# Kernel optimization log

Hardware: AMD Instinct MI355X
Metric: run time of the kernel (lower is better)

Reference implementation:

```python
import jax, jax.numpy as jnp
import numpy as np

B, S, I, H, C = 32, 512, 768, 512, 10


def setup_inputs() -> dict:
    key = jax.random.key(0)
    ks = jax.random.split(key, 16)
    n = lambda k, shp, s=0.02: jax.random.normal(k, shp, dtype=jnp.float32) * s
    inp = {
        "sentence_embeds": jax.random.normal(ks[0], (B, S, I), dtype=jnp.float32),
        "Wenc": n(ks[1], (H, I)),
        "benc": jnp.zeros((H,), jnp.float32),
        "Wdec": n(ks[2], (H, H)),
        "bdec": jnp.zeros((H,), jnp.float32),
        "v": jax.random.uniform(ks[3], (H,), dtype=jnp.float32),
        "Wih_f": n(ks[4], (4 * H, 2 * I)),
        "Whh_f": n(ks[5], (4 * H, H)),
        "bih_f": jnp.zeros((4 * H,), jnp.float32),
        "bhh_f": jnp.zeros((4 * H,), jnp.float32),
        "Wih_b": n(ks[6], (4 * H, 2 * I)),
        "Whh_b": n(ks[7], (4 * H, H)),
        "bih_b": jnp.zeros((4 * H,), jnp.float32),
        "bhh_b": jnp.zeros((4 * H,), jnp.float32),
        "Wout": n(ks[8], (C, 2 * H)),
        "bout": jnp.zeros((C,), jnp.float32),
    }
    return inp


def _run_direction(embeds, enc_proj, Wdec, bdec, v, Wih, Whh, bih, bhh):
    # embeds: [B,S,I], enc_proj: [B,S,H]. Returns per-step hidden states [S,B,H].
    b = embeds.shape[0]
    h0 = jnp.zeros((b, H), embeds.dtype)
    c0 = jnp.zeros((b, H), embeds.dtype)

    def step(carry, x_t):
        h, c = carry
        # Bahdanau additive attention over all encoder positions
        dec = h @ Wdec.T + bdec                                   # [B,H]
        scores = jnp.einsum("h,bsh->bs", v, jnp.tanh(enc_proj + dec[:, None, :]))
        w = jax.nn.softmax(scores, axis=1)                        # [B,S]
        ctx = jnp.einsum("bs,bsi->bi", w, embeds)                 # [B,I]
        inp = jnp.concatenate([ctx, x_t], axis=1)                 # [B,2I]
        gates = inp @ Wih.T + h @ Whh.T + (bih + bhh)             # [B,4H]
        i, f, g, o = jnp.split(gates, 4, axis=1)                  # torch LSTM gate order
        c = jax.nn.sigmoid(f) * c + jax.nn.sigmoid(i) * jnp.tanh(g)
        h = jax.nn.sigmoid(o) * jnp.tanh(c)
        return (h, c), h

    xs = jnp.swapaxes(embeds, 0, 1)  # [S,B,I]
    _, hs = jax.lax.scan(step, (h0, c0), xs)
    return hs


def reference(sentence_embeds, Wenc, benc, Wdec, bdec, v, Wih_f, Whh_f, bih_f, bhh_f,
              Wih_b, Whh_b, bih_b, bhh_b, Wout, bout):
    # Encoder projection is loop-invariant in the original; compute once.
    enc_proj = sentence_embeds @ Wenc.T + benc  # [B,S,H]
    hs_f = _run_direction(sentence_embeds, enc_proj, Wdec, bdec, v, Wih_f, Whh_f, bih_f, bhh_f)
    hs_b = _run_direction(sentence_embeds[:, ::-1, :], enc_proj, Wdec, bdec, v, Wih_b, Whh_b, bih_b, bhh_b)
    hs_b = hs_b[::-1]                                             # align backward outputs to time order
    combined = jnp.concatenate([hs_f, hs_b], axis=-1)             # [S,B,2H]
    preds = combined @ Wout.T + bout                              # [S,B,C]
    return jnp.swapaxes(preds, 0, 1)                              # [B,S,C]
```

## Files before the change

kernel.cpp:

```cpp
#include <hip/hip_runtime.h>
#include <stdint.h>

#define DEVINL __device__ __forceinline__

constexpr int B_  = 32;
constexpr int S_  = 512;
constexpr int I_  = 768;
constexpr int H_  = 512;
constexpr int C_  = 10;
constexpr int R_  = 64;
constexpr int G4H = 2048;
constexpr int I2_ = 1536;
constexpr int NBLK = 256;
constexpr int NTHR = 512;

using bf16x8 = __attribute__((ext_vector_type(8))) short;
using f32x4  = __attribute__((ext_vector_type(4))) float;
typedef unsigned short u16;
typedef unsigned int   u32;

constexpr size_t OFF_TE   = 0;
constexpr size_t OFF_EMB  = OFF_TE   + (size_t)B_*S_*H_*2;
constexpr size_t OFF_WDEC = OFF_EMB  + (size_t)B_*S_*I_*2;
constexpr size_t OFF_WHH  = OFF_WDEC + (size_t)H_*H_*2;
constexpr size_t OFF_WIL  = OFF_WHH  + (size_t)2*G4H*H_*2;
constexpr size_t OFF_WIR  = OFF_WIL  + (size_t)2*G4H*I_*2;
constexpr size_t OFF_WENC = OFF_WIR  + (size_t)2*G4H*I_*2;
constexpr size_t OFF_H    = OFF_WENC + (size_t)H_*I_*2;
constexpr size_t OFF_C    = OFF_H    + (size_t)R_*H_*2;
constexpr size_t OFF_TD   = OFF_C    + (size_t)R_*H_*4;
constexpr size_t OFF_HWH  = OFF_TD   + (size_t)R_*H_*4;
constexpr size_t OFF_XW   = OFF_HWH  + (size_t)R_*G4H*4;
constexpr size_t OFF_CTX  = OFF_XW   + (size_t)R_*G4H*4;
constexpr size_t OFF_SUME = OFF_CTX  + (size_t)R_*I_*4;
constexpr size_t OFF_M    = OFF_SUME + 256;
constexpr size_t OFF_BAR  = OFF_M    + 256;
constexpr int    BAR_W    = 64 + NBLK*32;
constexpr size_t WS_NEED  = OFF_BAR + BAR_W*4;

DEVINL float asf(u32 u){ union{u32 i; float f;} x; x.i=u; return x.f; }
DEVINL u32   asu(float f){ union{u32 i; float f;} x; x.f=f; return x.i; }
DEVINL float bf2f(u16 h){ return asf((u32)h << 16); }
DEVINL u16   f2bf(float f){ u32 u = asu(f); return (u16)((u + 0x7fffu + ((u>>16)&1u)) >> 16); }
DEVINL float frcp(float x){
#if __has_builtin(__builtin_amdgcn_rcpf)
  return __builtin_amdgcn_rcpf(x);
#else
  return 1.0f/x;
#endif
}
DEVINL float sigm(float x){ return frcp(1.0f + __expf(-x)); }

DEVINL float ldc_f(const float* p){ return __hip_atomic_load(p, __ATOMIC_RELAXED, __HIP_MEMORY_SCOPE_AGENT); }
DEVINL void  stc_f(float* p, float v){ __hip_atomic_store(p, v, __ATOMIC_RELAXED, __HIP_MEMORY_SCOPE_AGENT); }
DEVINL u32   ldc_u(const u32* p){ return __hip_atomic_load(p, __ATOMIC_RELAXED, __HIP_MEMORY_SCOPE_AGENT); }
DEVINL void  stc_u(u32* p, u32 v){ __hip_atomic_store(p, v, __ATOMIC_RELAXED, __HIP_MEMORY_SCOPE_AGENT); }
DEVINL void  addc_f(float* p, float v){ __hip_atomic_fetch_add(p, v, __ATOMIC_RELAXED, __HIP_MEMORY_SCOPE_AGENT); }

DEVINL void gridbar(u32* bar, u32 n){
  __syncthreads();
  if (threadIdx.x == 0)
    stc_u(&bar[64 + blockIdx.x*32], n);
  if (blockIdx.x == 0){
    if (threadIdx.x < NBLK){
      while (ldc_u(&bar[64 + threadIdx.x*32]) < n)
        __builtin_amdgcn_s_sleep(1);
    }
    __syncthreads();
    if (threadIdx.x == 0) stc_u(&bar[32], n);
  } else {
    if (threadIdx.x == 0){
      while (ldc_u(&bar[32]) < n)
        __builtin_amdgcn_s_sleep(1);
    }
  }
  __syncthreads();
}

DEVINL f32x4 gemm_h16(const u32* h32, size_t base, const u16 (*W)[520], int lr, int lkb){
  f32x4 acc = {0.f,0.f,0.f,0.f};
  #pragma unroll
  for (int half = 0; half < 2; ++half){
    u32 hreg[32];
    #pragma unroll
    for (int i2 = 0; i2 < 32; ++i2)
      hreg[i2] = ldc_u(h32 + base + half*128 + (i2>>2)*16 + (i2&3));
    #pragma unroll
    for (int ki = 0; ki < 8; ++ki){
      union { bf16x8 v; u32 w[4]; } ua;
      ua.w[0]=hreg[ki*4+0]; ua.w[1]=hreg[ki*4+1];
      ua.w[2]=hreg[ki*4+2]; ua.w[3]=hreg[ki*4+3];
      bf16x8 b = *(const bf16x8*)(&W[lr][(half*8+ki)*32 + lkb]);
      acc = __builtin_amdgcn_mfma_f32_16x16x32_bf16(ua.v, b, acc, 0, 0, 0);
    }
  }
  return acc;
}

struct SMemB { float ldsE[2][2][32]; float cpart[4][96][16]; };
struct SMemC { u16 Abuf[16][776]; float Gpre[32][16]; float Gs[32][16];
               float Hb[16][8]; float inv[16]; float sum[16]; };
union alignas(16) SMem { SMemB b; SMemC c; };

__global__ void k_setup(char* ws, const float* Wenc, const float* Wdec,
                        const float* Whh_f, const float* Whh_b,
                        const float* Wih_f, const float* Wih_b,
                        float* out){
  int tid = blockIdx.x*blockDim.x + threadIdx.x;
  int nth = gridDim.x*blockDim.x;
  for (int i = tid; i < B_*S_*C_; i += nth) out[i] = 0.f;
  u16* hB = (u16*)(ws+OFF_H);
  for (int i = tid; i < R_*H_; i += nth) hB[i] = 0;
  float* cS = (float*)(ws+OFF_C);
  for (int i = tid; i < R_*H_; i += nth) cS[i] = 0.f;
  float* mb = (float*)(ws+OFF_M);
  for (int i = tid; i < R_; i += nth) mb[i] = 0.f;
  u32* bar = (u32*)(ws+OFF_BAR);
  for (int i = tid; i < BAR_W; i += nth) bar[i] = 0u;
  u16* wd = (u16*)(ws+OFF_WDEC);
  for (int i = tid; i < H_*H_; i += nth) wd[i] = f2bf(Wdec[i]);
  u16* we = (u16*)(ws+OFF_WENC);
  for (int i = tid; i < H_*I_; i += nth) we[i] = f2bf(Wenc[i]);
  u16* wh = (u16*)(ws+OFF_WHH);
  for (int i = tid; i < G4H*H_; i += nth){
    wh[i] = f2bf(Whh_f[i]);
    wh[G4H*H_ + i] = f2bf(Whh_b[i]);
  }
  u16* wl = (u16*)(ws+OFF_WIL);
  u16* wr = (u16*)(ws+OFF_WIR);
  for (int i = tid; i < G4H*I_; i += nth){
    int n = i / I_, k = i - n*I_;
    wl[i]            = f2bf(Wih_f[n*I2_ + k]);
    wr[i]            = f2bf(Wih_f[n*I2_ + I_ + k]);
    wl[G4H*I_ + i]   = f2bf(Wih_b[n*I2_ + k]);
    wr[G4H*I_ + i]   = f2bf(Wih_b[n*I2_ + I_ + k]);
  }
}

__global__ void k_embconv(char* ws, const float* emb){
  u16* e = (u16*)(ws+OFF_EMB);
  int tid = blockIdx.x*blockDim.x + threadIdx.x;
  int nth = gridDim.x*blockDim.x;
  int n4 = (B_*S_*I_)/4;
  const float4* src = (const float4*)emb;
  ushort4* dst = (ushort4*)e;
  for (int i = tid; i < n4; i += nth){
    float4 x = src[i];
    ushort4 o;
    o.x = f2bf(x.x); o.y = f2bf(x.y); o.z = f2bf(x.z); o.w = f2bf(x.w);
    dst[i] = o;
  }
}

__global__ __launch_bounds__(256) void k_enc(char* ws, const float* benc){
  const u16* A = (const u16*)(ws+OFF_EMB);
  const u16* W = (const u16*)(ws+OFF_WENC);
  u16* Te = (u16*)(ws+OFF_TE);
  int wg = blockIdx.x;
  int mt = wg >> 3, ng = wg & 7;
  int wave = threadIdx.x >> 6, lane = threadIdx.x & 63;
  int m0 = mt*16, n0 = ng*64 + wave*16;
  int lr = lane & 15, lkb = (lane>>4)*8;
  const u16* ap = A + (size_t)(m0+lr)*I_ + lkb;
  const u16* bp = W + (size_t)(n0+lr)*I_ + lkb;
  f32x4 acc = {0.f,0.f,0.f,0.f};
  for (int k = 0; k < I_; k += 32){
    bf16x8 a = *(const bf16x8*)(ap + k);
    bf16x8 b = *(const bf16x8*)(bp + k);
    acc = __builtin_amdgcn_mfma_f32_16x16x32_bf16(a, b, acc, 0, 0, 0);
  }
  int row4 = (lane>>4)*4;
  #pragma unroll
  for (int q = 0; q < 4; q++){
    int rr = m0 + row4 + q, cc = n0 + lr;
    Te[(size_t)rr*H_ + cc] = f2bf(tanhf(acc[q] + benc[cc]));
  }
}

__global__ __launch_bounds__(NTHR) void k_persist(char* ws,
        const float* bdec, const float* v,
        const float* bih_f, const float* bhh_f,
        const float* bih_b, const float* bhh_b,
        const float* Wout, const float* bout, float* out){
  __shared__ SMem sh;
  __shared__ alignas(16) u16 wWhh[16][520];
  __shared__ alignas(16) u16 wWIR[16][776];
  __shared__ alignas(16) u16 wDec[16][520];
  __shared__ alignas(16) u16 wWIL[32][776];
  __shared__ float wOutL[10][8];
  __shared__ float bsumL[32];
  u32* bar = (u32*)(ws+OFF_BAR);
  u32 gen = 0;
  const int tid = threadIdx.x, lane = tid & 63, wave = tid >> 6;
  const int lr = lane & 15, lkb = (lane>>4)*8, row4 = (lane>>4)*4;
  const int blk = blockIdx.x;
  const int dirA = blk & 1, n0A = blk >> 1;
  const int ab   = blk & 31, pair = blk >> 5;
  const int s0A  = pair*32, s0B = S_ - pair*32 - 32;
  const int h0   = lane*8;
  const int cg   = (tid < 384) ? (tid % 96) : 0;
  const int rq   = (tid < 384) ? (tid / 96) : 0;
  const int dirC = blk >> 7, ncC = (blk >> 1) & 63, qbC = blk & 1;

  { const u16* src = (const u16*)(ws+OFF_WHH) + (size_t)dirA*G4H*H_ + (size_t)n0A*16*H_;
    for (int idx = tid; idx < 16*64; idx += NTHR){ int r = idx>>6, c8 = idx&63;
      *(uint4*)&wWhh[r][c8*8] = *(const uint4*)(src + (size_t)r*H_ + c8*8); } }
  { const u16* src = (const u16*)(ws+OFF_WIR) + (size_t)dirA*G4H*I_ + (size_t)n0A*16*I_;
    for (int idx = tid; idx < 16*96; idx += NTHR){ int r = idx/96, c8 = idx - r*96;
      *(uint4*)&wWIR[r][c8*8] = *(const uint4*)(src + (size_t)r*I_ + c8*8); } }
  if (blk < 32){
    const u16* src = (const u16*)(ws+OFF_WDEC) + (size_t)blk*16*H_;
    for (int idx = tid; idx < 16*64; idx += NTHR){ int r = idx>>6, c8 = idx&63;
      *(uint4*)&wDec[r][c8*8] = *(const uint4*)(src + (size_t)r*H_ + c8*8); } }
  { const u16* src = (const u16*)(ws+OFF_WIL) + (size_t)dirC*G4H*I_;
    for (int idx = tid; idx < 32*96; idx += NTHR){ int pr = idx/96, c8 = idx - pr*96;
      int g = pr>>3, j = pr&7;
      *(uint4*)&wWIL[pr][c8*8] = *(const uint4*)(src + (size_t)(g*512 + ncC*8 + j)*I_ + c8*8); } }
  { const float* bihp = dirC ? bih_b : bih_f;
    const float* bhhp = dirC ? bhh_b : bhh_f;
    if (tid < 32){ int g = tid>>3, c = tid&7; int n = g*512 + ncC*8 + c;
      bsumL[tid] = bihp[n] + bhhp[n]; }
    if (tid >= 64 && tid < 144){ int q = tid-64; int cc = q>>3, c = q&7;
      wOutL[cc][c] = Wout[(size_t)cc*1024 + dirC*512 + ncC*8 + c]; } }
  bf16x8 teR[8];
  { const u16* Te = (const u16*)(ws+OFF_TE);
    #pragma unroll
    for (int k = 0; k < 8; ++k){
      int r = wave + 8*k; int ci = r >> 5, u = r & 31;
      int s = (ci ? s0B : s0A) + u;
      teR[k] = *(const bf16x8*)(Te + ((size_t)(ab*S_ + s))*H_ + h0); } }
  bf16x8 embR[16];
  if (tid < 384){
    const u16* E = (const u16*)(ws+OFF_EMB);
    #pragma unroll
    for (int j = 0; j < 16; ++j){
      int r = rq*16 + j;
      int s = (r < 32) ? (s0A + r) : (s0B + (r - 32));
      embR[j] = *(const bf16x8*)(E + ((size_t)(ab*S_ + s))*I_ + cg*8); } }
  __syncthreads();

  for (int t = 0; t < S_; ++t){
    {
      const u32* h32 = (const u32*)(ws+OFF_H);
      if (wave < 2){
        int m0 = dirA*32 + wave*16;
        size_t base = (((size_t)(m0+lr))*H_ + lkb) >> 1;
        f32x4 acc = gemm_h16(h32, base, wWhh, lr, lkb);
        float* o = (float*)(ws+OFF_HWH);
        #pragma unroll
        for (int q = 0; q < 4; q++)
          stc_f(&o[(size_t)(m0 + row4 + q)*G4H + n0A*16 + lr], acc[q]);
      } else if (wave < 4){
        int bbase = (wave-2)*16;
        int trow = dirA ? (S_-1-t) : t;
        const u16* E = (const u16*)(ws+OFF_EMB);
        const u16* ap = E + ((size_t)(bbase+lr)*S_ + trow)*I_ + lkb;
        f32x4 acc = {0.f,0.f,0.f,0.f};
        for (int k = 0; k < I_; k += 32){
          bf16x8 a = *(const bf16x8*)(ap + k);
          bf16x8 b = *(const bf16x8*)(&wWIR[lr][k + lkb]);
          acc = __builtin_amdgcn_mfma_f32_16x16x32_bf16(a, b, acc, 0, 0, 0);
        }
        float* o = (float*)(ws+OFF_XW);
        #pragma unroll
        for (int q = 0; q < 4; q++)
          stc_f(&o[(size_t)(dirA*32 + bbase + row4 + q)*G4H + n0A*16 + lr], acc[q]);
      } else if (blk < 32){
        int m0 = (wave-4)*16;
        size_t base = (((size_t)(m0+lr))*H_ + lkb) >> 1;
        f32x4 acc = gemm_h16(h32, base, wDec, lr, lkb);
        float* Td = (float*)(ws+OFF_TD);
        #pragma unroll
        for (int q = 0; q < 4; q++){
          int rr = m0 + row4 + q, cc = blk*16 + lr;
          stc_f(&Td[rr*H_ + cc], tanhf(acc[q] + bdec[cc]));
        }
      } else {
        int zid = (((blk-32)<<2) + (wave-4))*64 + lane;
        float* ctx = (float*)(ws+OFF_CTX);
        if (zid < R_*I_) stc_f(&ctx[zid], 0.f);
        if (zid < R_) stc_f((float*)(ws+OFF_SUME) + zid, 0.f);
      }
    }
    gridbar(bar, ++gen);
    {
      const float* Td = (const float*)(ws+OFF_TD);
      const float* mbp = (const float*)(ws+OFF_M);
      float tdf[8], tdb[8], va[8];
      #pragma unroll
      for (int j = 0; j < 8; j++){
        tdf[j] = ldc_f(&Td[ab*H_ + h0 + j]);
        tdb[j] = ldc_f(&Td[(32+ab)*H_ + h0 + j]);
        va[j]  = v[h0 + j];
      }
      float mF = ldc_f(&mbp[ab]), mB = ldc_f(&mbp[32+ab]);
      #pragma unroll
      for (int k = 0; k < 8; ++k){
        int r = wave + 8*k;
        int ci = r >> 5, u = r & 31;
        bf16x8 tv = teR[k];
        float af = 0.f, ab2 = 0.f;
        #pragma unroll
        for (int j = 0; j < 8; ++j){
          float te = bf2f((u16)tv[j]);
          float df = fmaf(te, tdf[j], 1.0f);
          float db = fmaf(te, tdb[j], 1.0f);
          af  = fmaf((te+tdf[j])*frcp(df), va[j], af);
          ab2 = fmaf((te+tdb[j])*frcp(db), va[j], ab2);
        }
        #pragma unroll
        for (int off = 1; off < 64; off <<= 1){
          af  += __shfl_xor(af, off);
          ab2 += __shfl_xor(ab2, off);
        }
        float ef = __expf(fminf(fmaxf(af  - mF, -80.f), 80.f));
        float eb = __expf(fminf(fmaxf(ab2 - mB, -80.f), 80.f));
        if (lane == 0){ sh.b.ldsE[0][ci][u] = ef; sh.b.ldsE[1][ci][u] = eb; }
      }
      __syncthreads();
      if (tid < 2){
        float s = 0.f;
        for (int ci = 0; ci < 2; ci++)
          for (int u = 0; u < 32; u++) s += sh.b.ldsE[tid][ci][u];
        addc_f((float*)(ws+OFF_SUME) + tid*32 + ab, s);
      }
      if (tid < 384){
        const int ci = rq >> 1;
        float cf[8] = {0,0,0,0,0,0,0,0}, cb[8] = {0,0,0,0,0,0,0,0};
        #pragma unroll
        for (int j = 0; j < 16; ++j){
          int u = ((rq & 1) << 4) + j;
          float wf = sh.b.ldsE[0][ci][u];
          float wb = sh.b.ldsE[1][1-ci][31-u];
          bf16x8 e = embR[j];
          #pragma unroll
          for (int x = 0; x < 8; ++x){
            float ev = bf2f((u16)e[x]);
            cf[x] = fmaf(wf, ev, cf[x]);
            cb[x] = fmaf(wb, ev, cb[x]);
          }
        }
        #pragma unroll
        for (int x = 0; x < 8; ++x){
          sh.b.cpart[rq][cg][x]   = cf[x];
          sh.b.cpart[rq][cg][8+x] = cb[x];
        }
      }
      __syncthreads();
      {
        float* ctxg = (float*)(ws+OFF_CTX);
        for (int o = tid; o < 1536; o += NTHR){
          int d = (o >= 768) ? 1 : 0;
          int col = o - d*768;
          int cgx = col >> 3, c = col & 7;
          float s = sh.b.cpart[0][cgx][d*8+c] + sh.b.cpart[1][cgx][d*8+c]
                  + sh.b.cpart[2][cgx][d*8+c] + sh.b.cpart[3][cgx][d*8+c];
          addc_f(&ctxg[(size_t)(d*32+ab)*I_ + col], s);
        }
      }
    }
    gridbar(bar, ++gen);
    {
      const float* se = (const float*)(ws+OFF_SUME) + dirC*32 + qbC*16;
      if (tid < 16){
        float s_ = ldc_f(&se[tid]);
        sh.c.sum[tid] = s_;
        sh.c.inv[tid] = 1.0f / fmaxf(s_, 1e-30f);
      }
      __syncthreads();
      {
        const float* ctx = (const float*)(ws+OFF_CTX) + (size_t)(dirC*32 + qbC*16)*I_;
        float creg[24];
        int j = tid >> 5, k0 = (tid & 31) * 24;
        #pragma unroll
        for (int i2 = 0; i2 < 24; ++i2)
          creg[i2] = ldc_f(ctx + (size_t)j*I_ + k0 + i2);
        float inv = sh.c.inv[j];
        #pragma unroll
        for (int i2 = 0; i2 < 24; ++i2)
          sh.c.Abuf[j][k0 + i2] = f2bf(creg[i2] * inv);
      }
      __syncthreads();
      f32x4 acc = {0.f,0.f,0.f,0.f};
      if (wave < 2){
        for (int k = 0; k < I_; k += 32){
          bf16x8 av = *(const bf16x8*)(&sh.c.Abuf[lr][k + lkb]);
          bf16x8 bv = *(const bf16x8*)(&wWIL[wave*16 + lr][k + lkb]);
          acc = __builtin_amdgcn_mfma_f32_16x16x32_bf16(av, bv, acc, 0, 0, 0);
        }
      } else {
        const float* xW = (const float*)(ws+OFF_XW);
        const float* hW = (const float*)(ws+OFF_HWH);
        for (int ii = tid - 128; ii < 512; ii += 384){
          int pr = ii >> 4, j = ii & 15;
          int g = pr >> 3, c = pr & 7;
          int n = g*512 + ncC*8 + c;
          size_t rr = (size_t)(dirC*32 + qbC*16 + j);
          sh.c.Gpre[pr][j] = ldc_f(&xW[rr*G4H + n]) + ldc_f(&hW[rr*G4H + n]) + bsumL[pr];
        }
      }
      __syncthreads();
      if (wave < 2){
        int pr = wave*16 + lr;
        #pragma unroll
        for (int q = 0; q < 4; q++){
          int j = row4 + q;
          sh.c.Gs[pr][j] = acc[q] + sh.c.Gpre[pr][j];
        }
      }
      __syncthreads();
      float* cS = (float*)(ws+OFF_C);
      if (tid < 128){
        int j = tid >> 3, c = tid & 7;
        int hg = ncC*8 + c;
        size_t rr = (size_t)(dirC*32 + qbC*16 + j);
        float ig = sigm(sh.c.Gs[c][j]);
        float fg = sigm(sh.c.Gs[8+c][j]);
        float gg = tanhf(sh.c.Gs[16+c][j]);
        float og = sigm(sh.c.Gs[24+c][j]);
        float cn = fmaf(fg, cS[rr*H_ + hg], ig*gg);
        float hn = og * tanhf(cn);
        cS[rr*H_ + hg] = cn;
        sh.c.Hb[j][c] = hn;
      }
      __syncthreads();
      if (tid < 64){
        int j = tid >> 2, cp = tid & 3;
        size_t rr = (size_t)(dirC*32 + qbC*16 + j);
        u32 pk = (u32)f2bf(sh.c.Hb[j][cp*2]) | ((u32)f2bf(sh.c.Hb[j][cp*2+1]) << 16);
        stc_u((u32*)(ws+OFF_H) + ((rr*H_ + ncC*8) >> 1) + cp, pk);
      }
      if (tid < 160){
        int j = tid/10, cc = tid - j*10;
        float s = 0.f;
        #pragma unroll
        for (int c = 0; c < 8; c++) s = fmaf(sh.c.Hb[j][c], wOutL[cc][c], s);
        if (dirC == 0 && ncC == 0) s += bout[cc];
        int bb = qbC*16 + j;
        int st = dirC ? (S_-1-t) : t;
        atomicAdd(&out[((size_t)bb*S_ + st)*C_ + cc], s);
      }
      if (ncC == 0 && tid < 16){
        float* mp = (float*)(ws+OFF_M) + dirC*32 + qbC*16 + tid;
        stc_f(mp, ldc_f(mp) + logf(fmaxf(sh.c.sum[tid], 1e-30f)));
      }
    }
    gridbar(bar, ++gen);
  }
}

extern "C" void kernel_launch(void* const* d_in, const int* in_sizes, int n_in,
                              void* d_out, int out_size, void* d_ws, size_t ws_size,
                              hipStream_t stream){
  const float* emb   = (const float*)d_in[0];
  const float* Wenc  = (const float*)d_in[1];
  const float* benc  = (const float*)d_in[2];
  const float* Wdec  = (const float*)d_in[3];
  const float* bdec  = (const float*)d_in[4];
  const float* v     = (const float*)d_in[5];
  const float* Wih_f = (const float*)d_in[6];
  const float* Whh_f = (const float*)d_in[7];
  const float* bih_f = (const float*)d_in[8];
  const float* bhh_f = (const float*)d_in[9];
  const float* Wih_b = (const float*)d_in[10];
  const float* Whh_b = (const float*)d_in[11];
  const float* bih_b = (const float*)d_in[12];
  const float* bhh_b = (const float*)d_in[13];
  const float* Wout  = (const float*)d_in[14];
  const float* bout  = (const float*)d_in[15];
  float* out = (float*)d_out;
  char* ws = (char*)d_ws;
  if (ws_size < WS_NEED) return;

  k_setup<<<dim3(512), dim3(256), 0, stream>>>(ws, Wenc, Wdec, Whh_f, Whh_b, Wih_f, Wih_b, out);
  k_embconv<<<dim3(2048), dim3(256), 0, stream>>>(ws, emb);
  k_enc<<<dim3(8192), dim3(256), 0, stream>>>(ws, benc);
  k_persist<<<dim3(NBLK), dim3(NTHR), 0, stream>>>(ws, bdec, v,
      bih_f, bhh_f, bih_b, bhh_b, Wout, bout, out);
}
```

Baseline: 25.69 ms.

## Replace first grid barrier with per-producer flags and prefetch gate pre-activations

Removes the first grid-wide barrier of each timestep. Producer blocks now publish per-block generation flags (decoder tanh, context zeroing, gate partial products) through a shared-memory counter and a release store. Consumers spin only on the flags they need, and the xW/hW gate partials are fetched before the remaining grid barrier instead of after it. The context and sum zeroing moves to dedicated blocks with its own flag, and the initial zeroing moves into setup. The cost is extra spin loops and atomics, plus a risk of memory-ordering subtleties, since relaxed atomics are paired with a vmcnt drain.

Measured after the change: 26.38 ms. 1.03x slower.

```diff
diff --git a/kernel.cpp b/kernel.cpp
--- a/kernel.cpp
+++ b/kernel.cpp
@@ -36,7 +36,10 @@
 constexpr size_t OFF_M    = OFF_SUME + 256;
 constexpr size_t OFF_BAR  = OFF_M    + 256;
 constexpr int    BAR_W    = 64 + NBLK*32;
-constexpr size_t WS_NEED  = OFF_BAR + BAR_W*4;
+constexpr size_t OFF_DECF = OFF_BAR  + BAR_W*4;
+constexpr size_t OFF_ZF   = OFF_DECF + 32*32*4;
+constexpr size_t OFF_AF   = OFF_ZF   + 32*32*4;
+constexpr size_t WS_NEED  = OFF_AF + 256*32*4;
 
 DEVINL float asf(u32 u){ union{u32 i; float f;} x; x.i=u; return x.f; }
 DEVINL u32   asu(float f){ union{u32 i; float f;} x; x.f=f; return x.i; }
@@ -56,6 +59,7 @@
 DEVINL u32   ldc_u(const u32* p){ return __hip_atomic_load(p, __ATOMIC_RELAXED, __HIP_MEMORY_SCOPE_AGENT); }
 DEVINL void  stc_u(u32* p, u32 v){ __hip_atomic_store(p, v, __ATOMIC_RELAXED, __HIP_MEMORY_SCOPE_AGENT); }
 DEVINL void  addc_f(float* p, float v){ __hip_atomic_fetch_add(p, v, __ATOMIC_RELAXED, __HIP_MEMORY_SCOPE_AGENT); }
+DEVINL void vm_drain(){ asm volatile("s_waitcnt vmcnt(0)" ::: "memory"); }
 
 DEVINL void gridbar(u32* bar, u32 n){
   __syncthreads();
@@ -115,8 +119,14 @@
   for (int i = tid; i < R_*H_; i += nth) cS[i] = 0.f;
   float* mb = (float*)(ws+OFF_M);
   for (int i = tid; i < R_; i += nth) mb[i] = 0.f;
+  float* ctx = (float*)(ws+OFF_CTX);
+  for (int i = tid; i < R_*I_; i += nth) ctx[i] = 0.f;
+  float* se = (float*)(ws+OFF_SUME);
+  for (int i = tid; i < R_; i += nth) se[i] = 0.f;
   u32* bar = (u32*)(ws+OFF_BAR);
   for (int i = tid; i < BAR_W; i += nth) bar[i] = 0u;
+  u32* fl = (u32*)(ws+OFF_DECF);
+  for (int i = tid; i < (32+32+256)*32; i += nth) fl[i] = 0u;
   u16* wd = (u16*)(ws+OFF_WDEC);
   for (int i = tid; i < H_*H_; i += nth) wd[i] = f2bf(Wdec[i]);
   u16* we = (u16*)(ws+OFF_WENC);
@@ -189,7 +199,11 @@
   __shared__ alignas(16) u16 wWIL[32][776];
   __shared__ float wOutL[10][8];
   __shared__ float bsumL[32];
-  u32* bar = (u32*)(ws+OFF_BAR);
+  __shared__ u32 cntDec, cntZ, cntA;
+  u32* bar  = (u32*)(ws+OFF_BAR);
+  u32* decf = (u32*)(ws+OFF_DECF);
+  u32* zf   = (u32*)(ws+OFF_ZF);
+  u32* af   = (u32*)(ws+OFF_AF);
   u32 gen = 0;
   const int tid = threadIdx.x, lane = tid & 63, wave = tid >> 6;
   const int lr = lane & 15, lkb = (lane>>4)*8, row4 = (lane>>4)*4;
@@ -201,6 +215,8 @@
   const int cg   = (tid < 384) ? (tid % 96) : 0;
   const int rq   = (tid < 384) ? (tid / 96) : 0;
   const int dirC = blk >> 7, ncC = (blk >> 1) & 63, qbC = blk & 1;
+
+  if (tid == 0){ cntDec = 0u; cntZ = 0u; cntA = 0u; }
 
   { const u16* src = (const u16*)(ws+OFF_WHH) + (size_t)dirA*G4H*H_ + (size_t)n0A*16*H_;
     for (int idx = tid; idx < 16*64; idx += NTHR){ int r = idx>>6, c8 = idx&63;
@@ -240,6 +256,7 @@
   __syncthreads();
 
   for (int t = 0; t < S_; ++t){
+    const u32 tg = (u32)t + 1u;
     {
       const u32* h32 = (const u32*)(ws+OFF_H);
       if (wave < 2){
@@ -250,6 +267,11 @@
         #pragma unroll
         for (int q = 0; q < 4; q++)
           stc_f(&o[(size_t)(m0 + row4 + q)*G4H + n0A*16 + lr], acc[q]);
+        vm_drain();
+        if (lane == 0){
+          u32 old = atomicAdd(&cntA, 1u);
+          if (old == 4u*tg - 1u) stc_u(&af[blk*32], tg);
+        }
       } else if (wave < 4){
         int bbase = (wave-2)*16;
         int trow = dirA ? (S_-1-t) : t;
@@ -265,6 +287,11 @@
         #pragma unroll
         for (int q = 0; q < 4; q++)
           stc_f(&o[(size_t)(dirA*32 + bbase + row4 + q)*G4H + n0A*16 + lr], acc[q]);
+        vm_drain();
+        if (lane == 0){
+          u32 old = atomicAdd(&cntA, 1u);
+          if (old == 4u*tg - 1u) stc_u(&af[blk*32], tg);
+        }
       } else if (blk < 32){
         int m0 = (wave-4)*16;
         size_t base = (((size_t)(m0+lr))*H_ + lkb) >> 1;
@@ -275,14 +302,28 @@
           int rr = m0 + row4 + q, cc = blk*16 + lr;
           stc_f(&Td[rr*H_ + cc], tanhf(acc[q] + bdec[cc]));
         }
-      } else {
-        int zid = (((blk-32)<<2) + (wave-4))*64 + lane;
-        float* ctx = (float*)(ws+OFF_CTX);
-        if (zid < R_*I_) stc_f(&ctx[zid], 0.f);
-        if (zid < R_) stc_f((float*)(ws+OFF_SUME) + zid, 0.f);
-      }
-    }
-    gridbar(bar, ++gen);
+        vm_drain();
+        if (lane == 0){
+          u32 old = atomicAdd(&cntDec, 1u);
+          if (old == 4u*tg - 1u) stc_u(&decf[blk*32], tg);
+        }
+      } else if (blk < 64){
+        int z = blk - 32;
+        float* ctx = (float*)(ws+OFF_CTX) + (size_t)z*2*I_;
+        int q = (wave-4)*64 + lane;
+        #pragma unroll
+        for (int i2 = 0; i2 < 6; ++i2) stc_f(&ctx[q*6 + i2], 0.f);
+        if (q < 2) stc_f((float*)(ws+OFF_SUME) + z*2 + q, 0.f);
+        vm_drain();
+        if (lane == 0){
+          u32 old = atomicAdd(&cntZ, 1u);
+          if (old == 4u*tg - 1u) stc_u(&zf[z*32], tg);
+        }
+      }
+    }
+    if (lane < 32){
+      while (ldc_u(&decf[lane*32]) < tg) __builtin_amdgcn_s_sleep(1);
+    }
     {
       const float* Td = (const float*)(ws+OFF_TD);
       const float* mbp = (const float*)(ws+OFF_M);
@@ -299,31 +340,25 @@
         int r = wave + 8*k;
         int ci = r >> 5, u = r & 31;
         bf16x8 tv = teR[k];
-        float af = 0.f, ab2 = 0.f;
+        float af2 = 0.f, ab2 = 0.f;
         #pragma unroll
         for (int j = 0; j < 8; ++j){
           float te = bf2f((u16)tv[j]);
           float df = fmaf(te, tdf[j], 1.0f);
           float db = fmaf(te, tdb[j], 1.0f);
-          af  = fmaf((te+tdf[j])*frcp(df), va[j], af);
+          af2 = fmaf((te+tdf[j])*frcp(df), va[j], af2);
           ab2 = fmaf((te+tdb[j])*frcp(db), va[j], ab2);
         }
         #pragma unroll
         for (int off = 1; off < 64; off <<= 1){
-          af  += __shfl_xor(af, off);
+          af2 += __shfl_xor(af2, off);
           ab2 += __shfl_xor(ab2, off);
         }
-        float ef = __expf(fminf(fmaxf(af  - mF, -80.f), 80.f));
+        float ef = __expf(fminf(fmaxf(af2 - mF, -80.f), 80.f));
         float eb = __expf(fminf(fmaxf(ab2 - mB, -80.f), 80.f));
         if (lane == 0){ sh.b.ldsE[0][ci][u] = ef; sh.b.ldsE[1][ci][u] = eb; }
       }
       __syncthreads();
-      if (tid < 2){
-        float s = 0.f;
-        for (int ci = 0; ci < 2; ci++)
-          for (int u = 0; u < 32; u++) s += sh.b.ldsE[tid][ci][u];
-        addc_f((float*)(ws+OFF_SUME) + tid*32 + ab, s);
-      }
       if (tid < 384){
         const int ci = rq >> 1;
         float cf[8] = {0,0,0,0,0,0,0,0}, cb[8] = {0,0,0,0,0,0,0,0};
@@ -346,7 +381,16 @@
           sh.b.cpart[rq][cg][8+x] = cb[x];
         }
       }
-      __syncthreads();
+      if (lane < 32){
+        while (ldc_u(&zf[lane*32]) < tg) __builtin_amdgcn_s_sleep(1);
+      }
+      __syncthreads();
+      if (tid < 2){
+        float s = 0.f;
+        for (int ci = 0; ci < 2; ci++)
+          for (int u = 0; u < 32; u++) s += sh.b.ldsE[tid][ci][u];
+        addc_f((float*)(ws+OFF_SUME) + tid*32 + ab, s);
+      }
       {
         float* ctxg = (float*)(ws+OFF_CTX);
         for (int o = tid; o < 1536; o += NTHR){
@@ -359,6 +403,31 @@
         }
       }
     }
+    float pf0 = 0.f, pf1 = 0.f;
+    if (tid >= 128){
+      const float* xW = (const float*)(ws+OFF_XW);
+      const float* hW = (const float*)(ws+OFF_HWH);
+      {
+        int ii = tid - 128;
+        int pr = ii >> 4, j = ii & 15;
+        int g = pr >> 3, c = pr & 7;
+        int n = g*512 + ncC*8 + c;
+        int ablk = (g*32 + (ncC>>1))*2 + dirC;
+        while (ldc_u(&af[ablk*32]) < tg) __builtin_amdgcn_s_sleep(1);
+        size_t rr = (size_t)(dirC*32 + qbC*16 + j);
+        pf0 = ldc_f(&xW[rr*G4H + n]) + ldc_f(&hW[rr*G4H + n]);
+      }
+      int ii1 = (tid - 128) + 384;
+      if (ii1 < 512){
+        int pr = ii1 >> 4, j = ii1 & 15;
+        int g = pr >> 3, c = pr & 7;
+        int n = g*512 + ncC*8 + c;
+        int ablk = (g*32 + (ncC>>1))*2 + dirC;
+        while (ldc_u(&af[ablk*32]) < tg) __builtin_amdgcn_s_sleep(1);
+        size_t rr = (size_t)(dirC*32 + qbC*16 + j);
+        pf1 = ldc_f(&xW[rr*G4H + n]) + ldc_f(&hW[rr*G4H + n]);
+      }
+    }
     gridbar(bar, ++gen);
     {
       const float* se = (const float*)(ws+OFF_SUME) + dirC*32 + qbC*16;
@@ -389,14 +458,15 @@
           acc = __builtin_amdgcn_mfma_f32_16x16x32_bf16(av, bv, acc, 0, 0, 0);
         }
       } else {
-        const float* xW = (const float*)(ws+OFF_XW);
-        const float* hW = (const float*)(ws+OFF_HWH);
-        for (int ii = tid - 128; ii < 512; ii += 384){
+        {
+          int ii = tid - 128;
           int pr = ii >> 4, j = ii & 15;
-          int g = pr >> 3, c = pr & 7;
-          int n = g*512 + ncC*8 + c;
-          size_t rr = (size_t)(dirC*32 + qbC*16 + j);
-          sh.c.Gpre[pr][j] = ldc_f(&xW[rr*G4H + n]) + ldc_f(&hW[rr*G4H + n]) + bsumL[pr];
+          sh.c.Gpre[pr][j] = pf0 + bsumL[pr];
+        }
+        int ii1 = (tid - 128) + 384;
+        if (ii1 < 512){
+          int pr = ii1 >> 4, j = ii1 & 15;
+          sh.c.Gpre[pr][j] = pf1 + bsumL[pr];
         }
       }
       __syncthreads();
```
